# Optimization experiments

Hardware: AMD Instinct MI355X
Metric: run time of the kernel (lower is better)

The kernel has to match this reference:

```python
import jax, jax.numpy as jnp
import numpy as np
from jax import lax

DISP = 4   # max displacement for correlation -> 81 channels
KSZ = 3    # deform/gate conv kernel size


def conv2d(x, w, b=None):
    out = lax.conv_general_dilated(x, w, (1, 1), 'SAME',
                                   dimension_numbers=('NCHW', 'OIHW', 'NCHW'))
    if b is not None:
        out = out + b[None, :, None, None]
    return out


def correlation(x1, x2, d=DISP):
    # FlowNet-style cost volume, kernel_size=1: per-displacement channel-mean dot product.
    B, C, H, W = x1.shape
    x2p = jnp.pad(x2, ((0, 0), (0, 0), (d, d), (d, d)))
    outs = []
    for dy in range(2 * d + 1):
        for dx in range(2 * d + 1):
            shifted = lax.dynamic_slice(x2p, (0, 0, dy, dx), (B, C, H, W))
            outs.append(jnp.sum(x1 * shifted, axis=1) / C)
    return jnp.stack(outs, axis=1)  # [B, (2d+1)^2, H, W]


def bilinear_sample(img, y, x):
    # img: [B,C,H,W]; y,x: [B,H,W] float sample coords; zero padding outside.
    B, C, H, W = img.shape
    y0 = jnp.floor(y); x0 = jnp.floor(x)
    y1 = y0 + 1.0;     x1 = x0 + 1.0
    wy1 = y - y0; wx1 = x - x0
    wy0 = 1.0 - wy1; wx0 = 1.0 - wx1
    flat = img.reshape(B, C, H * W)

    def gather(yi, xi):
        valid = (yi >= 0) & (yi <= H - 1) & (xi >= 0) & (xi <= W - 1)
        yc = jnp.clip(yi, 0, H - 1).astype(jnp.int32)
        xc = jnp.clip(xi, 0, W - 1).astype(jnp.int32)
        idx = (yc * W + xc).reshape(B, 1, H * W)
        g = jnp.take_along_axis(flat, idx, axis=2).reshape(B, C, H, W)
        return g * valid.astype(img.dtype)[:, None]

    return (gather(y0, x0) * (wy0 * wx0)[:, None]
          + gather(y0, x1) * (wy0 * wx1)[:, None]
          + gather(y1, x0) * (wy1 * wx0)[:, None]
          + gather(y1, x1) * (wy1 * wx1)[:, None])


def deform_conv(img, offset, w, k=KSZ):
    # offset: [B, 2*k*k, H, W] with (dy, dx) pairs per kernel tap (row-major).
    B, C, H, W = img.shape
    pad = (k - 1) // 2
    ys = jnp.arange(H, dtype=img.dtype)[None, :, None]
    xs = jnp.arange(W, dtype=img.dtype)[None, None, :]
    out = jnp.zeros((B, w.shape[0], H, W), dtype=img.dtype)
    for kk in range(k * k):
        ky, kx = kk // k, kk % k
        y = ys + (ky - pad) + offset[:, 2 * kk]
        x = xs + (kx - pad) + offset[:, 2 * kk + 1]
        s = bilinear_sample(img, y, x)
        out = out + jnp.einsum('oc,bchw->bohw', w[:, :, ky, kx], s)
    return out


def linear_scale(x, std_multiplier=3.0):
    pos = x > 0
    cnt = jnp.sum(pos).astype(x.dtype)
    mean = jnp.sum(jnp.where(pos, x, 0.0)) / jnp.maximum(cnt, 1.0)
    var = jnp.sum(jnp.where(pos, (x - mean) ** 2, 0.0)) / jnp.maximum(cnt - 1.0, 1.0)
    ub = mean + std_multiplier * jnp.sqrt(var)
    ub = jnp.where(cnt >= 2.0, ub, 1.0)  # matches torch nan / empty-positive fallback
    return jnp.clip(x, 0.0, lax.stop_gradient(ub)) / ub


def setup_inputs() -> dict:
    key = jax.random.key(0)
    ks = jax.random.split(key, 10)
    B, C, H, W = 8, 256, 64, 64
    f = jnp.float32
    inp = {
        'inputs':   jax.random.normal(ks[0], (B, C, H, W), f),
        'in_state': jax.random.normal(ks[1], (B, C, H, W), f),
        'w_reset':  jax.random.normal(ks[2], (C, 2 * C, 3, 3), f) * 0.02,
        'b_reset':  jnp.zeros((C,), f),
        'w_update': jax.random.normal(ks[3], (C, 2 * C, 3, 3), f) * 0.02,
        'b_update': jnp.zeros((C,), f),
        'w_out':    jax.random.normal(ks[4], (C, 2 * C, 3, 3), f) * 0.02,
        'b_out':    jnp.zeros((C,), f),
        'w_offset': jax.random.normal(ks[5], (18, 81, 1, 1), f) * 0.01,
        'w_align':  jax.random.normal(ks[6], (C, C, 3, 3), f) * 0.01,
    }
    return inp


def reference(inputs, in_state, w_reset, b_reset, w_update, b_update,
              w_out, b_out, w_offset, w_align):
    # align_features: correlation -> 1x1 offset conv -> deformable conv
    corr = correlation(inputs, in_state)
    offset = conv2d(corr, w_offset)
    aligned = deform_conv(in_state, offset, w_align)
    # ConvGRU gates with linear-scaled relu gates
    stacked = jnp.concatenate([inputs, aligned], axis=1)
    update = linear_scale(jax.nn.relu(conv2d(stacked, w_update, b_update)))
    reset = linear_scale(jax.nn.relu(conv2d(stacked, w_reset, b_reset)))
    out_in = jax.nn.relu(conv2d(jnp.concatenate([inputs, in_state * reset], axis=1), w_out, b_out))
    new_state = in_state * (1.0 - update) + out_in * update
    return (new_state, new_state)  # (out_feat, new_state)
```

## Files before the change

kernel.cpp:

```cpp
#include <hip/hip_runtime.h>
#include <stdint.h>
#include <math.h>

typedef unsigned short u16;
typedef short bf16x8 __attribute__((ext_vector_type(8)));
typedef float f32x4 __attribute__((ext_vector_type(4)));

#define MFMA16x16x32(a,b,c) __builtin_amdgcn_mfma_f32_16x16x32_bf16((a),(b),(c),0,0,0)

typedef __attribute__((address_space(3))) void as3_void;
typedef const __attribute__((address_space(1))) void as1_void;

__device__ __forceinline__ void g2l16(const void* g, void* l){
#if __has_builtin(__builtin_amdgcn_global_load_lds)
  __builtin_amdgcn_global_load_lds((as1_void*)g, (as3_void*)l, 16, 0, 0);
#else
  *(int4*)l = *(const int4*)g;
#endif
}

__device__ __forceinline__ u16 f2bf(float f){
  uint32_t u = __builtin_bit_cast(uint32_t, f);
  u += 0x7fffu + ((u >> 16) & 1u);
  return (u16)(u >> 16);
}
__device__ __forceinline__ float bf2f(u16 h){
  uint32_t u = ((uint32_t)h) << 16;
  return __builtin_bit_cast(float, u);
}
__device__ __forceinline__ void unpack8(int4 v, float* o){
  uint32_t w0=(uint32_t)v.x, w1=(uint32_t)v.y, w2=(uint32_t)v.z, w3=(uint32_t)v.w;
  o[0]=__builtin_bit_cast(float, w0<<16); o[1]=__builtin_bit_cast(float, w0&0xffff0000u);
  o[2]=__builtin_bit_cast(float, w1<<16); o[3]=__builtin_bit_cast(float, w1&0xffff0000u);
  o[4]=__builtin_bit_cast(float, w2<<16); o[5]=__builtin_bit_cast(float, w2&0xffff0000u);
  o[6]=__builtin_bit_cast(float, w3<<16); o[7]=__builtin_bit_cast(float, w3&0xffff0000u);
}
__device__ __forceinline__ int iclampi(int v,int lo,int hi){ return v<lo?lo:(v>hi?hi:v); }

__global__ void k_repack(const float* __restrict__ w_reset, const float* __restrict__ b_reset,
                         const float* __restrict__ w_update, const float* __restrict__ b_update,
                         const float* __restrict__ w_out, const float* __restrict__ w_offset,
                         const float* __restrict__ w_align,
                         u16* __restrict__ wgate, u16* __restrict__ wout,
                         u16* __restrict__ walign, float* __restrict__ woff,
                         float* __restrict__ biascat){
  int idx = blockIdx.x * 256 + threadIdx.x;
  if (idx < 512*4608){
    int e = idx & 7, j = (idx >> 3) & 2047, chunk = idx >> 14;
    int nb = chunk & 1, kk = chunk >> 1;
    int l = j & 15, q = (j >> 4) & 3, t16 = (j >> 6) & 15, ks2 = j >> 10;
    int n = nb*256 + t16*16 + l;
    int tap = kk >> 3, ksin = kk & 7;
    int c = ksin*64 + ks2*32 + q*8 + e;
    int ky = tap/3, kx = tap%3;
    float v = (n < 256) ? w_update[((n*512 + c)*3 + ky)*3 + kx]
                        : w_reset[(((n-256)*512 + c)*3 + ky)*3 + kx];
    wgate[idx] = f2bf(v);
  }
  if (idx < 256*4608){
    int e = idx & 7, j = (idx >> 3) & 1023, chunk = idx >> 13;
    int nb = chunk & 1, kk = chunk >> 1;
    int l = j & 15, q = (j >> 4) & 3, t8 = (j >> 6) & 7, ks2 = j >> 9;
    int n = nb*128 + t8*16 + l;
    int tap = kk >> 3, ksin = kk & 7;
    int c = ksin*64 + ks2*32 + q*8 + e;
    int ky = tap/3, kx = tap%3;
    wout[idx] = f2bf(w_out[((n*512 + c)*3 + ky)*3 + kx]);
  }
  if (idx < 256*2304){
    int n = idx / 2304, k = idx % 2304;
    int tap = k >> 8, c = k & 255;
    int ky = tap/3, kx = tap%3;
    walign[idx] = f2bf(w_align[((n*256 + c)*3 + ky)*3 + kx]);
  }
  if (idx < 1458) woff[idx] = w_offset[idx] * (1.f/256.f);
  if (idx < 512) biascat[idx] = (idx < 256) ? b_update[idx] : b_reset[idx-256];
}

__global__ __launch_bounds__(256) void k_transform(const float* __restrict__ inputs,
    const float* __restrict__ in_state, u16* __restrict__ stacked,
    u16* __restrict__ stacked2, u16* __restrict__ x2pad){
  __shared__ u16 t1[64*264];
  __shared__ u16 t2[64*264];
  int tid = threadIdx.x, bh = blockIdx.x;
  int b = bh >> 6, h = bh & 63;
  int w = tid & 63, cq = tid >> 6;
  for (int i = 0; i < 64; ++i){
    int c = i*4 + cq;
    int gi = ((b*256 + c)*64 + h)*64 + w;
    t1[w*264 + c] = f2bf(inputs[gi]);
    t2[w*264 + c] = f2bf(in_state[gi]);
  }
  __syncthreads();
  int px = tid >> 2, cg = tid & 3;
#pragma unroll
  for (int u = 0; u < 8; ++u){
    int c = cg*64 + u*8;
    int4 v1 = *(const int4*)(t1 + px*264 + c);
    int4 v2 = *(const int4*)(t2 + px*264 + c);
    *(int4*)(stacked  + (((b*66 + h+1)*66) + (px+1))*512 + c) = v1;
    *(int4*)(stacked2 + (((b*66 + h+1)*66) + (px+1))*512 + c) = v1;
    *(int4*)(x2pad    + (((b*72 + h+4)*72) + (px+4))*256 + c) = v2;
  }
}

__global__ __launch_bounds__(256) void k_corr(const u16* __restrict__ stacked,
    const u16* __restrict__ x2pad, float* __restrict__ corr){
  __shared__ u16 lA[8192];
  __shared__ u16 lB[32768];
  int tid = threadIdx.x, idx = blockIdx.x;
  int b = idx >> 6, ty = (idx >> 3) & 7, tx = idx & 7;
  int h0 = ty*8, w0 = tx*8;
  int wave = tid >> 6, lane = tid & 63, l15 = lane & 15, quad = lane >> 4;
  f32x4 acc[4][4];
#pragma unroll
  for (int i=0;i<4;i++)
#pragma unroll
    for (int j=0;j<4;j++){ f32x4 z = {0.f,0.f,0.f,0.f}; acc[i][j] = z; }

  for (int s = 0; s < 2; ++s){
#pragma unroll
    for (int i = 0; i < 4; ++i){
      int j = tid + i*256;
      int ml = j & 15, q = (j>>4)&3, mt = (j>>6)&3, ks = j >> 8;
      int px = mt*16 + ml, py = px >> 3, pxx = px & 7;
      const u16* g = stacked + (((b*66 + h0+py+1)*66) + (w0+pxx+1))*512 + s*128 + ks*32 + q*8;
      g2l16(g, lA + j*8);
    }
#pragma unroll
    for (int i = 0; i < 16; ++i){
      int j = tid + i*256;
      int nl = j & 15, q = (j>>4)&3, nt = (j>>6)&15, ks = j >> 10;
      int qp = nt*16 + nl, qy = qp >> 4, qx = qp & 15;
      const u16* g = x2pad + (((b*72 + h0+qy)*72) + (w0+qx))*256 + s*128 + ks*32 + q*8;
      g2l16(g, lB + j*8);
    }
    __syncthreads();
#pragma unroll
    for (int ks = 0; ks < 4; ++ks){
      bf16x8 bv[4];
#pragma unroll
      for (int ni=0; ni<4; ++ni){
        int nt = wave*4 + ni;
        bv[ni] = *(const bf16x8*)(lB + (((ks*16 + nt)*4 + quad)*16 + l15)*8);
      }
#pragma unroll
      for (int mi=0; mi<4; ++mi){
        bf16x8 av = *(const bf16x8*)(lA + (((ks*4 + mi)*4 + quad)*16 + l15)*8);
#pragma unroll
        for (int ni=0; ni<4; ++ni) acc[mi][ni] = MFMA16x16x32(av, bv[ni], acc[mi][ni]);
      }
    }
    __syncthreads();
  }
#pragma unroll
  for (int mi=0; mi<4; ++mi){
#pragma unroll
    for (int ni=0; ni<4; ++ni){
      int n = wave*64 + ni*16 + l15;
      int qy = n >> 4, qx = n & 15;
#pragma unroll
      for (int r=0; r<4; ++r){
        int m = mi*16 + quad*4 + r;
        int py = m >> 3, pxx = m & 7;
        int dy = qy - py, dx = qx - pxx;
        if ((unsigned)dy <= 8u && (unsigned)dx <= 8u)
          corr[(((b*64 + h0+py)*64) + (w0+pxx))*81 + dy*9 + dx] = acc[mi][ni][r];
      }
    }
  }
}

__global__ __launch_bounds__(256) void k_offset(const float* __restrict__ corr,
    const float* __restrict__ woff, float* __restrict__ offs){
  __shared__ float lc[32*84];
  __shared__ float lw[18*84];
  int tid = threadIdx.x, blk = blockIdx.x;
  int row = blk >> 1, half = blk & 1;
  int base = row*5184 + half*32*81;
  for (int i = tid; i < 32*81; i += 256){
    int px = i / 81, d = i % 81;
    lc[px*84 + d] = corr[base + i];
  }
  for (int i = tid; i < 18*84; i += 256){
    int o = i / 84, d = i % 84;
    if (d < 81) lw[i] = woff[o*81 + d];
  }
  __syncthreads();
  int px = tid & 31, og = tid >> 5;
  for (int o = og; o < 18; o += 8){
    float s = 0.f;
#pragma unroll
    for (int dd = 0; dd < 20; ++dd){
      float4 a = *(const float4*)(lc + px*84 + dd*4);
      float4 wv = *(const float4*)(lw + o*84 + dd*4);
      s += a.x*wv.x + a.y*wv.y + a.z*wv.z + a.w*wv.w;
    }
    s += lc[px*84 + 80] * lw[o*84 + 80];
    offs[(row*64 + half*32 + px)*18 + o] = s;
  }
}

__global__ __launch_bounds__(256) void k_deform(const u16* __restrict__ x2pad,
    const float* __restrict__ offs, const u16* __restrict__ walign,
    u16* __restrict__ stacked){
  __shared__ u16 lA[16384];
  int tid = threadIdx.x, bh = blockIdx.x;
  int b = bh >> 6, h = bh & 63;
  int wave = tid >> 6, lane = tid & 63, l15 = lane & 15, quad = lane >> 4;
  int px = tid >> 2, cg = tid & 3;
  int mt_s = px >> 4, ml_s = px & 15;
  f32x4 acc[4][4];
#pragma unroll
  for (int i=0;i<4;i++)
#pragma unroll
    for (int j=0;j<4;j++){ f32x4 z = {0.f,0.f,0.f,0.f}; acc[i][j] = z; }

  for (int tap = 0; tap < 9; ++tap){
    int ky = tap/3, kx = tap%3;
    float offy = offs[(bh*64 + px)*18 + 2*tap];
    float offx = offs[(bh*64 + px)*18 + 2*tap + 1];
    float y = (float)(h + ky - 1) + offy;
    float x = (float)(px + kx - 1) + offx;
    float y0f = floorf(y), x0f = floorf(x);
    float wy1 = y - y0f, wx1 = x - x0f;
    float wy0 = 1.f - wy1, wx0 = 1.f - wx1;
    int iy0 = iclampi((int)y0f, -4, 67), ix0 = iclampi((int)x0f, -4, 67);
    int iy1 = iclampi((int)y0f + 1, -4, 67), ix1 = iclampi((int)x0f + 1, -4, 67);
    const u16* p00 = x2pad + (((b*72 + iy0+4)*72) + (ix0+4))*256 + cg*64;
    const u16* p01 = x2pad + (((b*72 + iy0+4)*72) + (ix1+4))*256 + cg*64;
    const u16* p10 = x2pad + (((b*72 + iy1+4)*72) + (ix0+4))*256 + cg*64;
    const u16* p11 = x2pad + (((b*72 + iy1+4)*72) + (ix1+4))*256 + cg*64;
    float w00 = wy0*wx0, w01 = wy0*wx1, w10 = wy1*wx0, w11 = wy1*wx1;
#pragma unroll
    for (int u = 0; u < 8; ++u){
      int4 v00 = *(const int4*)(p00 + u*8);
      int4 v01 = *(const int4*)(p01 + u*8);
      int4 v10 = *(const int4*)(p10 + u*8);
      int4 v11 = *(const int4*)(p11 + u*8);
      float a00[8], a01[8], a10[8], a11[8];
      unpack8(v00,a00); unpack8(v01,a01); unpack8(v10,a10); unpack8(v11,a11);
      union { u16 h2[8]; int4 v; } R;
#pragma unroll
      for (int jj = 0; jj < 8; ++jj)
        R.h2[jj] = f2bf(w00*a00[jj] + w01*a01[jj] + w10*a10[jj] + w11*a11[jj]);
      int ch = cg*64 + u*8;
      int ks = ch >> 5, q = (ch >> 3) & 3;
      *(int4*)(lA + (((ks*4 + mt_s)*4 + q)*16 + ml_s)*8) = R.v;
    }
    __syncthreads();
#pragma unroll
    for (int ks = 0; ks < 8; ++ks){
      bf16x8 bv[4];
#pragma unroll
      for (int ni=0; ni<4; ++ni){
        int n = wave*64 + ni*16 + l15;
        bv[ni] = *(const bf16x8*)(walign + n*2304 + tap*256 + ks*32 + quad*8);
      }
#pragma unroll
      for (int mi=0; mi<4; ++mi){
        bf16x8 av = *(const bf16x8*)(lA + (((ks*4 + mi)*4 + quad)*16 + l15)*8);
#pragma unroll
        for (int ni=0; ni<4; ++ni) acc[mi][ni] = MFMA16x16x32(av, bv[ni], acc[mi][ni]);
      }
    }
    __syncthreads();
  }
#pragma unroll
  for (int mi=0; mi<4; ++mi){
#pragma unroll
    for (int ni=0; ni<4; ++ni){
      int n = wave*64 + ni*16 + l15;
#pragma unroll
      for (int r=0; r<4; ++r){
        int m = mi*16 + quad*4 + r;
        stacked[(((b*66 + h+1)*66) + (m+1))*512 + 256 + n] = f2bf(acc[mi][ni][r]);
      }
    }
  }
}

template<int NT, bool STATS>
__global__ __launch_bounds__(512, 2) void k_conv256(const u16* __restrict__ in,
    const u16* __restrict__ wts, const float* __restrict__ bias,
    u16* __restrict__ outp, float* __restrict__ partials){
  constexpr int NI = NT / 4;
  constexpr int BLOADS = NT / 4;
  __shared__ u16 lA[2][16384];
  __shared__ u16 lB[2][NT*1024];

  int tid = threadIdx.x, g = blockIdx.x;
  int work = (g & 7) * 32 + (g >> 3);
  int nb = work >> 7, mt = work & 127;
  int b = mt >> 4, h0 = (mt & 15) * 4;
  int wave = tid >> 6, lane = tid & 63, l15 = lane & 15, quad = lane >> 4;
  int wm = wave & 1, wn = wave >> 1;

  f32x4 acc[8][NI];
#pragma unroll
  for (int i=0;i<8;i++)
#pragma unroll
    for (int j=0;j<NI;j++){ f32x4 z = {0.f,0.f,0.f,0.f}; acc[i][j] = z; }

  auto STAGE = [&](int d, int kk){
    int tap = kk >> 3, ksin = kk & 7;
    int ky = tap/3, kx = tap - ky*3;
    const u16* abase = in + ((b*66 + h0 + ky)*66 + kx)*512 + ksin*64;
#pragma unroll
    for (int i = 0; i < 4; ++i){
      int j = tid + i*512;
      int l = j & 15, q = (j >> 4) & 3, t16 = (j >> 6) & 15, ks2 = j >> 10;
      int px = t16*16 + l, r = px >> 6, w = px & 63;
      g2l16(abase + (r*66 + w)*512 + ks2*32 + q*8, &lA[d][j*8]);
    }
    const u16* wch = wts + (size_t)(kk*2 + nb) * (NT*1024);
#pragma unroll
    for (int i = 0; i < BLOADS; ++i){
      int j = tid + i*512;
      g2l16(wch + j*8, &lB[d][j*8]);
    }
  };

  STAGE(0, 0);
  STAGE(1, 1);

#pragma unroll 2
  for (int t = 0; t < 72; ++t){
    int cur = t & 1;
    if (t < 71){
      if constexpr (NT == 16) asm volatile("s_waitcnt vmcnt(8)" ::: "memory");
      else                    asm volatile("s_waitcnt vmcnt(6)" ::: "memory");
    } else {
      asm volatile("s_waitcnt vmcnt(0)" ::: "memory");
    }
    __builtin_amdgcn_s_barrier();
    asm volatile("" ::: "memory");

    const u16* A = &lA[cur][0];
    const u16* B = &lB[cur][0];
    bf16x8 bv[2][NI];
#pragma unroll
    for (int ks2 = 0; ks2 < 2; ++ks2)
#pragma unroll
      for (int ni = 0; ni < NI; ++ni){
        int nt = wn*NI + ni;
        bv[ks2][ni] = *(const bf16x8*)(B + (((ks2*NT + nt)*4 + quad)*16 + l15)*8);
      }
    __builtin_amdgcn_s_setprio(1);
#pragma unroll
    for (int mi = 0; mi < 8; ++mi){
      int mrow = wm*8 + mi;
#pragma unroll
      for (int ks2 = 0; ks2 < 2; ++ks2){
        bf16x8 av = *(const bf16x8*)(A + (((ks2*16 + mrow)*4 + quad)*16 + l15)*8);
#pragma unroll
        for (int ni = 0; ni < NI; ++ni)
          acc[mi][ni] = MFMA16x16x32(av, bv[ks2][ni], acc[mi][ni]);
      }
    }
    __builtin_amdgcn_s_setprio(0);

    asm volatile("" ::: "memory");
    __builtin_amdgcn_s_barrier();
    asm volatile("" ::: "memory");
    if (t + 2 < 72) STAGE(cur, t + 2);
  }

  float bvl[NI];
#pragma unroll
  for (int ni = 0; ni < NI; ++ni)
    bvl[ni] = bias[nb*(NT*16) + wn*(NI*16) + ni*16 + l15];
  float sc = 0.f, ss = 0.f, sq = 0.f;
#pragma unroll
  for (int mi=0; mi<8; ++mi){
#pragma unroll
    for (int ni=0; ni<NI; ++ni){
      int n = nb*(NT*16) + wn*(NI*16) + ni*16 + l15;
#pragma unroll
      for (int r=0; r<4; ++r){
        int m = wm*128 + mi*16 + quad*4 + r;
        int row = h0 + (m >> 6), w = m & 63;
        float v = acc[mi][ni][r] + bvl[ni];
        v = fmaxf(v, 0.f);
        outp[(((b*64 + row)*64) + w)*(NT*32) + n] = f2bf(v);
        if (STATS){ sc += (v > 0.f) ? 1.f : 0.f; ss += v; sq += v*v; }
      }
    }
  }
  if constexpr (STATS){
    __shared__ float red[8][3];
#pragma unroll
    for (int off = 32; off; off >>= 1){
      sc += __shfl_down(sc, off); ss += __shfl_down(ss, off); sq += __shfl_down(sq, off);
    }
    if (lane == 0){ red[wave][0]=sc; red[wave][1]=ss; red[wave][2]=sq; }
    __syncthreads();
    if (tid == 0){
      float a0=0,a1=0,a2=0;
      for (int w2=0; w2<8; ++w2){ a0+=red[w2][0]; a1+=red[w2][1]; a2+=red[w2][2]; }
      partials[work*3+0]=a0; partials[work*3+1]=a1; partials[work*3+2]=a2;
    }
  }
}

__global__ __launch_bounds__(256) void k_finalize(const float* __restrict__ partials,
                                                  float* __restrict__ ubs){
  __shared__ float red[4][6];
  int tid = threadIdx.x, lane = tid & 63, wave = tid >> 6;
  float cu=0,su=0,qu=0,cr=0,sr=0,qr=0;
  {
    float c = partials[tid*3+0], s = partials[tid*3+1], q = partials[tid*3+2];
    if (tid < 128){ cu=c; su=s; qu=q; } else { cr=c; sr=s; qr=q; }
  }
#pragma unroll
  for (int off = 32; off; off >>= 1){
    cu += __shfl_down(cu, off); su += __shfl_down(su, off); qu += __shfl_down(qu, off);
    cr += __shfl_down(cr, off); sr += __shfl_down(sr, off); qr += __shfl_down(qr, off);
  }
  if (lane == 0){ red[wave][0]=cu; red[wave][1]=su; red[wave][2]=qu;
                  red[wave][3]=cr; red[wave][4]=sr; red[wave][5]=qr; }
  __syncthreads();
  if (tid < 2){
    double C=0, S=0, Q=0;
    for (int w2=0; w2<4; ++w2){
      C += red[w2][tid*3+0]; S += red[w2][tid*3+1]; Q += red[w2][tid*3+2];
    }
    float ub = 1.f;
    if (C >= 2.0){
      double mean = S / C;
      double var = (Q - C*mean*mean) / (C - 1.0);
      if (var < 0.0) var = 0.0;
      ub = (float)(mean + 3.0*sqrt(var));
    }
    ubs[tid] = ub;
    ubs[2+tid] = 1.f/ub;
  }
}

__global__ __launch_bounds__(256) void k_mulreset(const u16* __restrict__ G,
    const u16* __restrict__ x2pad, const float* __restrict__ ubs,
    u16* __restrict__ stacked2){
  int tid = threadIdx.x, bh = blockIdx.x;
  int b = bh >> 6, h = bh & 63;
  int px = tid >> 2, cg = tid & 3;
  float ubr = ubs[1], inv = ubs[3];
#pragma unroll
  for (int u = 0; u < 8; ++u){
    int c = cg*64 + u*8;
    int4 gv = *(const int4*)(G + (bh*64 + px)*512 + 256 + c);
    int4 sv = *(const int4*)(x2pad + (((b*72 + h+4)*72) + (px+4))*256 + c);
    float gf[8], sf[8]; unpack8(gv, gf); unpack8(sv, sf);
    union { u16 h2[8]; int4 v; } R;
#pragma unroll
    for (int j=0;j<8;j++){
      float r = fminf(gf[j], ubr) * inv;
      R.h2[j] = f2bf(sf[j] * r);
    }
    *(int4*)(stacked2 + (((b*66 + h+1)*66) + (px+1))*512 + 256 + c) = R.v;
  }
}

__global__ __launch_bounds__(256) void k_final(const u16* __restrict__ G,
    const u16* __restrict__ O, const float* __restrict__ in_state,
    const float* __restrict__ ubs, float* __restrict__ dout){
  __shared__ float Q[64*65];
  __shared__ float P[64*65];
  int tid = threadIdx.x, bh = blockIdx.x;
  int b = bh >> 6, h = bh & 63;
  float ubu = ubs[0], inv = ubs[2];
  int px = tid >> 2, cs = (tid & 3)*16;
  int w = tid & 63, c4 = tid >> 6;
  for (int cb = 0; cb < 4; ++cb){
#pragma unroll
    for (int tt = 0; tt < 2; ++tt){
      int cl = cs + tt*8;
      int c = cb*64 + cl;
      int4 gv = *(const int4*)(G + (bh*64 + px)*512 + c);
      int4 ov = *(const int4*)(O + (bh*64 + px)*256 + c);
      float gf[8], of[8]; unpack8(gv, gf); unpack8(ov, of);
#pragma unroll
      for (int j=0;j<8;j++){
        float u = fminf(gf[j], ubu) * inv;
        Q[px*65 + cl + j] = u;
        P[px*65 + cl + j] = of[j]*u;
      }
    }
    __syncthreads();
    for (int i = 0; i < 16; ++i){
      int cl = i*4 + c4;
      int c = cb*64 + cl;
      int gidx = (((b*256 + c)*64) + h)*64 + w;
      float s = in_state[gidx];
      float v = s*(1.f - Q[w*65 + cl]) + P[w*65 + cl];
      dout[gidx] = v;
      dout[8388608 + gidx] = v;
    }
    __syncthreads();
  }
}

extern "C" void kernel_launch(void* const* d_in, const int* in_sizes, int n_in,
                              void* d_out, int out_size, void* d_ws, size_t ws_size,
                              hipStream_t stream){
  (void)in_sizes; (void)n_in; (void)out_size; (void)ws_size;
  const float* inputs   = (const float*)d_in[0];
  const float* in_state = (const float*)d_in[1];
  const float* w_reset  = (const float*)d_in[2];
  const float* b_reset  = (const float*)d_in[3];
  const float* w_update = (const float*)d_in[4];
  const float* b_update = (const float*)d_in[5];
  const float* w_out    = (const float*)d_in[6];
  const float* b_out    = (const float*)d_in[7];
  const float* w_offset = (const float*)d_in[8];
  const float* w_align  = (const float*)d_in[9];
  float* dout = (float*)d_out;

  char* ws = (char*)d_ws;
  size_t off = 0;
  auto alloc = [&](size_t bytes)->char*{
    char* p = ws + off; off = (off + bytes + 255) & ~(size_t)255; return p;
  };
  const size_t x2pad_b   = 8ull*72*72*256*2;
  const size_t stacked_b = 8ull*66*66*512*2;
  u16* x2pad    = (u16*)alloc(x2pad_b);
  u16* stacked  = (u16*)alloc(stacked_b);
  u16* stacked2 = (u16*)alloc(stacked_b);
  float* corr   = (float*)alloc(8ull*64*64*81*4);
  float* offs   = (float*)alloc(8ull*64*64*18*4);
  u16* G        = (u16*)alloc(8ull*64*64*512*2);
  u16* O        = (u16*)alloc(8ull*64*64*256*2);
  u16* wgate    = (u16*)alloc(512ull*4608*2);
  u16* woutb    = (u16*)alloc(256ull*4608*2);
  u16* walignb  = (u16*)alloc(256ull*2304*2);
  float* woff   = (float*)alloc(1458*4);
  float* biascat= (float*)alloc(512*4);
  float* partials=(float*)alloc(1024*3*4);
  float* ubs    = (float*)alloc(4*4);

  hipMemsetAsync(x2pad,    0, x2pad_b,   stream);
  hipMemsetAsync(stacked,  0, stacked_b, stream);
  hipMemsetAsync(stacked2, 0, stacked_b, stream);

  k_repack<<<9216, 256, 0, stream>>>(w_reset, b_reset, w_update, b_update, w_out,
                                     w_offset, w_align, wgate, woutb, walignb, woff, biascat);
  k_transform<<<512, 256, 0, stream>>>(inputs, in_state, stacked, stacked2, x2pad);
  k_corr<<<512, 256, 0, stream>>>(stacked, x2pad, corr);
  k_offset<<<1024, 256, 0, stream>>>(corr, woff, offs);
  k_deform<<<512, 256, 0, stream>>>(x2pad, offs, walignb, stacked);
  k_conv256<16, true><<<256, 512, 0, stream>>>(stacked, wgate, biascat, G, partials);
  k_finalize<<<1, 256, 0, stream>>>(partials, ubs);
  k_mulreset<<<512, 256, 0, stream>>>(G, x2pad, ubs, stacked2);
  k_conv256<8, false><<<256, 512, 0, stream>>>(stacked2, woutb, b_out, O, nullptr);
  k_final<<<512, 256, 0, stream>>>(G, O, in_state, ubs, dout);
}
```

Baseline: 688.6 us.

## Interleave staged half-tile loads with MFMA phases in conv256 main loop

Measured after the change: 701.9 us. Within noise of the previous version (+1.9%).

```diff
diff --git a/kernel.cpp b/kernel.cpp
--- a/kernel.cpp
+++ b/kernel.cpp
@@ -280,12 +280,85 @@
   }
 }
 
+__device__ __forceinline__ void stageA_half(u16* __restrict__ dst,
+    const u16* __restrict__ in, int b, int h0, int kk, int hh, int tid){
+  int tap = kk >> 3, ksin = kk & 7;
+  int ky = tap/3, kx = tap - ky*3;
+  const u16* abase = in + ((b*66 + h0 + ky)*66 + kx)*512 + ksin*64;
+#pragma unroll
+  for (int i = 0; i < 2; ++i){
+    int pi = (tid >> 8)*2 + i;
+    int ks2 = pi >> 1, blk = pi & 1;
+    int j = (ks2<<10) | (blk<<9) | (hh<<8) | (tid & 255);
+    int l = j & 15, q = (j >> 4) & 3;
+    int t16 = ((j >> 6) & 3) | (hh<<2) | (blk<<3);
+    int px = t16*16 + l, r = px >> 6, w = px & 63;
+    g2l16(abase + (r*66 + w)*512 + ks2*32 + q*8, dst + j*8);
+  }
+}
+__device__ __forceinline__ void stageB16_half(u16* __restrict__ dst,
+    const u16* __restrict__ wts, int nb, int kk, int hh, int tid){
+  const u16* wch = wts + (size_t)(kk*2 + nb) * 16384;
+#pragma unroll
+  for (int i = 0; i < 2; ++i){
+    int j = (i<<10) | ((tid>>7)<<8) | (hh<<7) | (tid & 127);
+    g2l16(wch + j*8, dst + j*8);
+  }
+}
+__device__ __forceinline__ void stageB8(u16* __restrict__ dst,
+    const u16* __restrict__ wts, int nb, int kk, int tid){
+  const u16* wch = wts + (size_t)(kk*2 + nb) * 8192;
+#pragma unroll
+  for (int i = 0; i < 2; ++i){
+    int j = (i<<9) | tid;
+    g2l16(wch + j*8, dst + j*8);
+  }
+}
+
+#define PHASE(QM, QN, WV, STG_STMT) do { \
+  bf16x8 av_[4][2], bv_[2][2]; \
+  _Pragma("unroll") \
+  for (int m4=0;m4<4;++m4){ \
+    _Pragma("unroll") \
+    for (int k2=0;k2<2;++k2){ \
+      int mrow = wm*8 + (QM)*4 + m4; \
+      av_[m4][k2] = *(const bf16x8*)(Acur + (((k2*16 + mrow)*4 + quad)*16 + l15)*8); \
+    } } \
+  _Pragma("unroll") \
+  for (int n2=0;n2<2;++n2){ \
+    _Pragma("unroll") \
+    for (int k2=0;k2<2;++k2){ \
+      int ntl = wn*NI + (QN)*2 + n2; \
+      bv_[n2][k2] = *(const bf16x8*)(Bcur + (((k2*NT + ntl)*4 + quad)*16 + l15)*8); \
+    } } \
+  STG_STMT; \
+  asm volatile("" ::: "memory"); \
+  __builtin_amdgcn_s_barrier(); \
+  asm volatile("s_waitcnt lgkmcnt(0)" ::: "memory"); \
+  __builtin_amdgcn_sched_barrier(0); \
+  __builtin_amdgcn_s_setprio(1); \
+  _Pragma("unroll") \
+  for (int k2=0;k2<2;++k2){ \
+    _Pragma("unroll") \
+    for (int m4=0;m4<4;++m4){ \
+      _Pragma("unroll") \
+      for (int n2=0;n2<2;++n2){ \
+        acc[(QM)*4+m4][(QN)*2+n2] = \
+          MFMA16x16x32(av_[m4][k2], bv_[n2][k2], acc[(QM)*4+m4][(QN)*2+n2]); \
+      } } } \
+  __builtin_amdgcn_s_setprio(0); \
+  __builtin_amdgcn_sched_barrier(0); \
+  if (hasnext) { asm volatile("s_waitcnt vmcnt(" #WV ")" ::: "memory"); } \
+  else         { asm volatile("s_waitcnt vmcnt(0)" ::: "memory"); } \
+  asm volatile("" ::: "memory"); \
+  __builtin_amdgcn_s_barrier(); \
+} while(0)
+
 template<int NT, bool STATS>
 __global__ __launch_bounds__(512, 2) void k_conv256(const u16* __restrict__ in,
     const u16* __restrict__ wts, const float* __restrict__ bias,
     u16* __restrict__ outp, float* __restrict__ partials){
   constexpr int NI = NT / 4;
-  constexpr int BLOADS = NT / 4;
   __shared__ u16 lA[2][16384];
   __shared__ u16 lB[2][NT*1024];
 
@@ -302,68 +375,40 @@
 #pragma unroll
     for (int j=0;j<NI;j++){ f32x4 z = {0.f,0.f,0.f,0.f}; acc[i][j] = z; }
 
-  auto STAGE = [&](int d, int kk){
-    int tap = kk >> 3, ksin = kk & 7;
-    int ky = tap/3, kx = tap - ky*3;
-    const u16* abase = in + ((b*66 + h0 + ky)*66 + kx)*512 + ksin*64;
-#pragma unroll
-    for (int i = 0; i < 4; ++i){
-      int j = tid + i*512;
-      int l = j & 15, q = (j >> 4) & 3, t16 = (j >> 6) & 15, ks2 = j >> 10;
-      int px = t16*16 + l, r = px >> 6, w = px & 63;
-      g2l16(abase + (r*66 + w)*512 + ks2*32 + q*8, &lA[d][j*8]);
-    }
-    const u16* wch = wts + (size_t)(kk*2 + nb) * (NT*1024);
-#pragma unroll
-    for (int i = 0; i < BLOADS; ++i){
-      int j = tid + i*512;
-      g2l16(wch + j*8, &lB[d][j*8]);
-    }
-  };
-
-  STAGE(0, 0);
-  STAGE(1, 1);
-
-#pragma unroll 2
+  if constexpr (NT == 16){
+    stageA_half(&lA[0][0], in, b, h0, 0, 0, tid);
+    stageB16_half(&lB[0][0], wts, nb, 0, 0, tid);
+    stageA_half(&lA[0][0], in, b, h0, 0, 1, tid);
+    stageB16_half(&lB[0][0], wts, nb, 0, 1, tid);
+    asm volatile("s_waitcnt vmcnt(4)" ::: "memory");
+  } else {
+    stageA_half(&lA[0][0], in, b, h0, 0, 0, tid);
+    stageB8(&lB[0][0], wts, nb, 0, tid);
+    stageA_half(&lA[0][0], in, b, h0, 0, 1, tid);
+    asm volatile("s_waitcnt vmcnt(2)" ::: "memory");
+  }
+  asm volatile("" ::: "memory");
+  __builtin_amdgcn_s_barrier();
+
+#pragma unroll 1
   for (int t = 0; t < 72; ++t){
-    int cur = t & 1;
-    if (t < 71){
-      if constexpr (NT == 16) asm volatile("s_waitcnt vmcnt(8)" ::: "memory");
-      else                    asm volatile("s_waitcnt vmcnt(6)" ::: "memory");
+    int d = t & 1;
+    const u16* Acur = &lA[d][0];
+    const u16* Bcur = &lB[d][0];
+    u16* Anext = &lA[d^1][0];
+    u16* Bnext = &lB[d^1][0];
+    bool hasnext = (t < 71);
+    int kn = t + 1;
+    if constexpr (NT == 16){
+      PHASE(0,0,2, if (hasnext) stageA_half(Anext, in, b, h0, kn, 0, tid));
+      PHASE(0,1,6, if (hasnext) stageB16_half(Bnext, wts, nb, kn, 0, tid));
+      PHASE(1,0,6, if (hasnext) stageA_half(Anext, in, b, h0, kn, 1, tid));
+      PHASE(1,1,4, if (hasnext) stageB16_half(Bnext, wts, nb, kn, 1, tid));
     } else {
-      asm volatile("s_waitcnt vmcnt(0)" ::: "memory");
-    }
-    __builtin_amdgcn_s_barrier();
-    asm volatile("" ::: "memory");
-
-    const u16* A = &lA[cur][0];
-    const u16* B = &lB[cur][0];
-    bf16x8 bv[2][NI];
-#pragma unroll
-    for (int ks2 = 0; ks2 < 2; ++ks2)
-#pragma unroll
-      for (int ni = 0; ni < NI; ++ni){
-        int nt = wn*NI + ni;
-        bv[ks2][ni] = *(const bf16x8*)(B + (((ks2*NT + nt)*4 + quad)*16 + l15)*8);
-      }
-    __builtin_amdgcn_s_setprio(1);
-#pragma unroll
-    for (int mi = 0; mi < 8; ++mi){
-      int mrow = wm*8 + mi;
-#pragma unroll
-      for (int ks2 = 0; ks2 < 2; ++ks2){
-        bf16x8 av = *(const bf16x8*)(A + (((ks2*16 + mrow)*4 + quad)*16 + l15)*8);
-#pragma unroll
-        for (int ni = 0; ni < NI; ++ni)
-          acc[mi][ni] = MFMA16x16x32(av, bv[ks2][ni], acc[mi][ni]);
-      }
-    }
-    __builtin_amdgcn_s_setprio(0);
-
-    asm volatile("" ::: "memory");
-    __builtin_amdgcn_s_barrier();
-    asm volatile("" ::: "memory");
-    if (t + 2 < 72) STAGE(cur, t + 2);
+      PHASE(0,0,4, if (hasnext){ stageA_half(Anext, in, b, h0, kn, 0, tid);
+                                 stageB8(Bnext, wts, nb, kn, tid); });
+      PHASE(1,0,2, if (hasnext) stageA_half(Anext, in, b, h0, kn, 1, tid));
+    }
   }
 
   float bvl[NI];
```
